# Kernel tuning notes

Measured on AMD Instinct MI355X. Metric: run time of the kernel, lower is better.

The kernel has to match this reference:

```python
import math
import jax, jax.numpy as jnp
import numpy as np

N_HEADS = 16

def setup_inputs() -> dict:
    key = jax.random.key(0)
    k1, k2, k3 = jax.random.split(key, 3)
    B, T, C = 4, 2048, 1024
    alpha = 0.5
    std = alpha * (1.0 / C) ** 0.5
    x = jax.random.normal(k1, (B, T, C), dtype=jnp.float32)
    w_attn = jax.random.normal(k2, (C, 3 * C), dtype=jnp.float32) * std
    b_attn = jnp.zeros((3 * C,), dtype=jnp.float32)
    w_proj = jax.random.normal(k3, (C, C), dtype=jnp.float32) * std
    b_proj = jnp.zeros((C,), dtype=jnp.float32)
    return {"x": x, "w_attn": w_attn, "b_attn": b_attn, "w_proj": w_proj, "b_proj": b_proj}

def reference(x, w_attn, b_attn, w_proj, b_proj):
    B, T, C = x.shape
    H = N_HEADS
    D = C // H
    qkv = x @ w_attn + b_attn                      # [B,T,3C]
    q, k, v = jnp.split(qkv, 3, axis=-1)
    # [B,T,C] -> [B,H,T,D]
    q = q.reshape(B, T, H, D).transpose(0, 2, 1, 3)
    k = k.reshape(B, T, H, D).transpose(0, 2, 1, 3)
    v = v.reshape(B, T, H, D).transpose(0, 2, 1, 3)
    att = jnp.einsum('bhqd,bhkd->bhqk', q, k) * (1.0 / math.sqrt(D))
    causal = jnp.tril(jnp.ones((T, T), dtype=bool))
    att = jnp.where(causal, att, -jnp.inf)
    att = jax.nn.softmax(att, axis=-1)
    y = jnp.einsum('bhqk,bhkd->bhqd', att, v)      # [B,H,T,D]
    y = y.transpose(0, 2, 1, 3).reshape(B, T, C)
    return y @ w_proj + b_proj
```

## Files before the change

kernel.cpp:

```cpp
#include <hip/hip_runtime.h>
#include <hip/hip_bf16.h>

typedef __bf16 bf16x8 __attribute__((ext_vector_type(8)));
typedef float f32x4 __attribute__((ext_vector_type(4)));
typedef unsigned short u16x8 __attribute__((ext_vector_type(8)));
typedef unsigned short u16x4 __attribute__((ext_vector_type(4)));

#define HB 16
#define TT 2048
#define CCH 1024
#define DD 64

#define AS1 __attribute__((address_space(1)))
#define AS3 __attribute__((address_space(3)))
#define GL16(gp, lp) __builtin_amdgcn_global_load_lds((const AS1 void*)(gp), (AS3 void*)(lp), 16, 0, 0)

__device__ __forceinline__ unsigned short f2bf(float f) {
  union { __hip_bfloat16 h; unsigned short u; } cv;
  cv.h = __float2bfloat16(f);
  return cv.u;
}

__device__ __forceinline__ unsigned pack2(float lo, float hi) {
  return (unsigned)f2bf(lo) | ((unsigned)f2bf(hi) << 16);
}

__device__ __forceinline__ f32x4 mfma16(bf16x8 a, bf16x8 b, f32x4 c) {
  return __builtin_amdgcn_mfma_f32_16x16x32_bf16(a, b, c, 0, 0, 0);
}


__global__ __launch_bounds__(256) void cvt_f32_bf16(const float* __restrict__ in,
                                                    unsigned short* __restrict__ out,
                                                    int n4) {
  int i = blockIdx.x * 256 + threadIdx.x;
  if (i >= n4) return;
  float4 v = reinterpret_cast<const float4*>(in)[i];
  u16x4 o;
  o.x = f2bf(v.x); o.y = f2bf(v.y); o.z = f2bf(v.z); o.w = f2bf(v.w);
  *reinterpret_cast<u16x4*>(out + (size_t)i * 4) = o;
}

__global__ __launch_bounds__(256) void transpose_cvt(const float* __restrict__ w,
                                                     unsigned short* __restrict__ wt,
                                                     int N) {
  __shared__ unsigned short t[32][33];
  int nb = blockIdx.x * 32, kb = blockIdx.y * 32;
  int tx = threadIdx.x & 31, ty = threadIdx.x >> 5;
  #pragma unroll
  for (int r = 0; r < 32; r += 8)
    t[ty + r][tx] = f2bf(w[(size_t)(kb + ty + r) * N + nb + tx]);
  __syncthreads();
  #pragma unroll
  for (int r = 0; r < 32; r += 8)
    wt[(size_t)(nb + ty + r) * 1024 + kb + tx] = t[tx][ty + r];
}


template <int EPI>
__global__ __launch_bounds__(256) void gemm_bf16(
    const unsigned short* __restrict__ A,
    const unsigned short* __restrict__ Bt,
    const float* __restrict__ bias,
    float* __restrict__ outf,
    unsigned short* __restrict__ qb,
    unsigned short* __restrict__ kb,
    unsigned short* __restrict__ vt) {
  __shared__ unsigned short As[8192];
  __shared__ unsigned short Bs[8192];
  const int tid = threadIdx.x;
  const int lane = tid & 63;
  const int wid = tid >> 6;
  const int r16 = lane & 15, g = lane >> 4;
  const int wm = wid >> 1, wn = wid & 1;
  const int m0 = blockIdx.y * 128, n0 = blockIdx.x * 128;
  const int srow = tid >> 3;
  const int schx = (tid & 7) ^ (srow & 7);

  f32x4 acc[4][4];
  #pragma unroll
  for (int i = 0; i < 4; ++i)
    #pragma unroll
    for (int j = 0; j < 4; ++j) acc[i][j] = (f32x4){0.f, 0.f, 0.f, 0.f};

  const int rx = r16 & 7;

  for (int kt = 0; kt < 1024; kt += 64) {
    #pragma unroll
    for (int i = 0; i < 4; ++i) {
      const int row = i * 32 + srow;
      GL16(A + (size_t)(m0 + row) * 1024 + kt + schx * 8, As + i * 2048 + tid * 8);
    }
    #pragma unroll
    for (int i = 0; i < 4; ++i) {
      const int row = i * 32 + srow;
      GL16(Bt + (size_t)(n0 + row) * 1024 + kt + schx * 8, Bs + i * 2048 + tid * 8);
    }
    __syncthreads();
    #pragma unroll
    for (int h = 0; h < 2; ++h) {
      bf16x8 af[4], bfr[4];
      #pragma unroll
      for (int i = 0; i < 4; ++i)
        af[i] = *reinterpret_cast<const bf16x8*>(
            &As[(wm * 64 + i * 16 + r16) * 64 + ((g + 4 * h) ^ rx) * 8]);
      #pragma unroll
      for (int j = 0; j < 4; ++j)
        bfr[j] = *reinterpret_cast<const bf16x8*>(
            &Bs[(wn * 64 + j * 16 + r16) * 64 + ((g + 4 * h) ^ rx) * 8]);
      #pragma unroll
      for (int i = 0; i < 4; ++i)
        #pragma unroll
        for (int j = 0; j < 4; ++j)
          acc[i][j] = mfma16(af[i], bfr[j], acc[i][j]);
    }
    __syncthreads();
  }

  #pragma unroll
  for (int i = 0; i < 4; ++i) {
    #pragma unroll
    for (int j = 0; j < 4; ++j) {
      const int n = n0 + wn * 64 + j * 16 + r16;
      const int mbase = m0 + wm * 64 + i * 16 + g * 4;
      const float bi = bias[n];
      if (EPI == 1) {
        #pragma unroll
        for (int r = 0; r < 4; ++r)
          outf[(size_t)(mbase + r) * 1024 + n] = acc[i][j][r] + bi;
      } else {
        const int which = n >> 10;
        const int cc2 = n & 1023;
        const int h = cc2 >> 6, d = cc2 & 63;
        const int b = mbase >> 11, t = mbase & 2047;
        if (which == 2) {
          u16x4 o;
          #pragma unroll
          for (int r = 0; r < 4; ++r) o[r] = f2bf(acc[i][j][r] + bi);
          *reinterpret_cast<u16x4*>(
              &vt[(((size_t)b * HB + h) * DD + d) * TT + t]) = o;
        } else {
          unsigned short* dst = (which == 0) ? qb : kb;
          const float sc = (which == 0) ? 0.18033688011112042f : 1.0f;
          #pragma unroll
          for (int r = 0; r < 4; ++r)
            dst[(((size_t)b * HB + h) * TT + (t + r)) * DD + d] =
                f2bf((acc[i][j][r] + bi) * sc);
        }
      }
    }
  }
}


__global__ __launch_bounds__(512, 2) void attn_kernel(
    const unsigned short* __restrict__ qg_,
    const unsigned short* __restrict__ kg_,
    const unsigned short* __restrict__ vtg_,
    unsigned short* __restrict__ yb) {
  const int bh = blockIdx.y;
  const int jb = blockIdx.x;
  const int tid = threadIdx.x;
  const int wid = tid >> 6;
  const int lane = tid & 63;
  const int r16 = lane & 15, g = lane >> 4;
  const unsigned short* Q = qg_ + (size_t)bh * TT * DD;
  const unsigned short* K = kg_ + (size_t)bh * TT * DD;
  const unsigned short* Vt = vtg_ + (size_t)bh * DD * TT;
  const int b = bh >> 4, h = bh & 15;

  __shared__ unsigned short smem[2][16384];

  const int krow0 = tid >> 3;
  const int kchx = (tid & 7) ^ (krow0 & 7);
  const int vd0 = tid >> 4;
  const int vchx = (tid & 15) ^ (vd0 & 7);
  const int rx = r16 & 7;

#define STAGE(bi, kvb_) do {                                                      \
    unsigned short* sb_ = &smem[bi][0];                                           \
    const unsigned short* gk_ = K + (size_t)(kvb_) * DD;                          \
    GL16(gk_ + (size_t)krow0 * DD + kchx * 8,              sb_ + tid * 8);        \
    GL16(gk_ + (size_t)(64 + krow0) * DD + kchx * 8,       sb_ + 4096 + tid * 8); \
    GL16(Vt + (size_t)vd0 * TT + (kvb_) + vchx * 8,        sb_ + 8192 + tid * 8); \
    GL16(Vt + (size_t)(32 + vd0) * TT + (kvb_) + vchx * 8, sb_ + 12288 + tid * 8);\
  } while (0)

  #pragma unroll
  for (int part = 0; part < 2; ++part) {
    const int qg0 = (part == 0) ? jb * 128 : (15 - jb) * 128;
    const int nt = (part == 0) ? (jb + 1) : (16 - jb);
    const int qw = qg0 + wid * 16;
    const int q = qw + r16;

    bf16x8 qf0 = *reinterpret_cast<const bf16x8*>(&Q[(size_t)q * DD + g * 8]);
    bf16x8 qf1 = *reinterpret_cast<const bf16x8*>(&Q[(size_t)q * DD + 32 + g * 8]);

    f32x4 yacc[4];
    #pragma unroll
    for (int db = 0; db < 4; ++db) yacc[db] = (f32x4){0.f, 0.f, 0.f, 0.f};
    float m = -1e30f, l = 0.f;

    STAGE(0, qg0 * 0);
    if (nt > 1) {
      STAGE(1, 128);
      asm volatile("s_waitcnt vmcnt(4)" ::: "memory");
    } else {
      asm volatile("s_waitcnt vmcnt(0)" ::: "memory");
    }
    __builtin_amdgcn_s_barrier();

    for (int t = 0; t < nt; ++t) {
      const int kvb = t * 128;
      const unsigned short* sK = &smem[t & 1][0];
      const unsigned short* sV = &smem[t & 1][8192];

      float s[8][4];
      #pragma unroll
      for (int c = 0; c < 8; ++c) {
        bf16x8 kfa = *reinterpret_cast<const bf16x8*>(
            &sK[(c * 16 + r16) * 64 + (g ^ rx) * 8]);
        bf16x8 kfb = *reinterpret_cast<const bf16x8*>(
            &sK[(c * 16 + r16) * 64 + ((g + 4) ^ rx) * 8]);
        f32x4 z = (f32x4){0.f, 0.f, 0.f, 0.f};
        z = mfma16(kfa, qf0, z);
        z = mfma16(kfb, qf1, z);
        #pragma unroll
        for (int r = 0; r < 4; ++r) s[c][r] = z[r];
      }

      float mx = -1e30f;
      if (t == nt - 1) {
        #pragma unroll
        for (int c = 0; c < 8; ++c)
          #pragma unroll
          for (int r = 0; r < 4; ++r) {
            if (kvb + c * 16 + 4 * g + r > q) s[c][r] = -1e30f;
            mx = fmaxf(mx, s[c][r]);
          }
      } else {
        #pragma unroll
        for (int c = 0; c < 8; ++c)
          #pragma unroll
          for (int r = 0; r < 4; ++r) mx = fmaxf(mx, s[c][r]);
      }
      mx = fmaxf(mx, __shfl_xor(mx, 16));
      mx = fmaxf(mx, __shfl_xor(mx, 32));

      if (!__all(mx <= m + 8.f)) {
        const float mn = fmaxf(m, mx);
        const float al = exp2f(m - mn);
        m = mn;
        l *= al;
        #pragma unroll
        for (int db = 0; db < 4; ++db)
          #pragma unroll
          for (int r = 0; r < 4; ++r) yacc[db][r] *= al;
      }
      float rs = 0.f;
      #pragma unroll
      for (int c = 0; c < 8; ++c)
        #pragma unroll
        for (int r = 0; r < 4; ++r) {
          s[c][r] = exp2f(s[c][r] - m);
          rs += s[c][r];
        }
      rs += __shfl_xor(rs, 16);
      rs += __shfl_xor(rs, 32);
      l += rs;

      const int s0l = r16 + 16 * ((2 * g) & 3);
      const int s1l = r16 + 16 * ((2 * g + 1) & 3);
      #pragma unroll
      for (int kk = 0; kk < 4; ++kk) {
        const unsigned x0 = pack2(s[2 * kk][0], s[2 * kk][1]);
        const unsigned x1 = pack2(s[2 * kk][2], s[2 * kk][3]);
        const unsigned y0 = pack2(s[2 * kk + 1][0], s[2 * kk + 1][1]);
        const unsigned y1 = pack2(s[2 * kk + 1][2], s[2 * kk + 1][3]);
        unsigned a0 = __shfl((int)x0, s0l, 64);
        unsigned b0 = __shfl((int)y0, s0l, 64);
        unsigned a1 = __shfl((int)x1, s0l, 64);
        unsigned b1 = __shfl((int)y1, s0l, 64);
        unsigned a2 = __shfl((int)x0, s1l, 64);
        unsigned b2 = __shfl((int)y0, s1l, 64);
        unsigned a3 = __shfl((int)x1, s1l, 64);
        unsigned b3 = __shfl((int)y1, s1l, 64);
        union { unsigned w[4]; bf16x8 v; } pf;
        pf.w[0] = (g < 2) ? a0 : b0;
        pf.w[1] = (g < 2) ? a1 : b1;
        pf.w[2] = (g < 2) ? a2 : b2;
        pf.w[3] = (g < 2) ? a3 : b3;
        #pragma unroll
        for (int db = 0; db < 4; ++db) {
          bf16x8 vf = *reinterpret_cast<const bf16x8*>(
              &sV[(db * 16 + r16) * 128 + ((kk * 4 + g) ^ rx) * 8]);
          yacc[db] = mfma16(vf, pf.v, yacc[db]);
        }
      }

      __syncthreads();
      if (t + 2 < nt) STAGE(t & 1, (t + 2) * 128);
    }

    const float rl = 1.0f / l;
    #pragma unroll
    for (int db = 0; db < 4; ++db) {
      u16x4 o;
      #pragma unroll
      for (int r = 0; r < 4; ++r) o[r] = f2bf(yacc[db][r] * rl);
      *reinterpret_cast<u16x4*>(
          &yb[((size_t)b * TT + q) * CCH + h * DD + db * 16 + 4 * g]) = o;
    }
  }
#undef STAGE
}


extern "C" void kernel_launch(void* const* d_in, const int* in_sizes, int n_in,
                              void* d_out, int out_size, void* d_ws, size_t ws_size,
                              hipStream_t stream) {
  const float* x      = (const float*)d_in[0];
  const float* w_attn = (const float*)d_in[1];
  const float* b_attn = (const float*)d_in[2];
  const float* w_proj = (const float*)d_in[3];
  const float* b_proj = (const float*)d_in[4];
  float* out = (float*)d_out;
  char* ws = (char*)d_ws;

  unsigned short* xb  = (unsigned short*)(ws + 0);
  unsigned short* wat = (unsigned short*)(ws + 16777216);
  unsigned short* wpt = (unsigned short*)(ws + 23068672);
  unsigned short* qb  = (unsigned short*)(ws + 25165824);
  unsigned short* kb  = (unsigned short*)(ws + 41943040);
  unsigned short* vt  = (unsigned short*)(ws + 58720256);
  unsigned short* yb  = (unsigned short*)(ws + 75497472);

  cvt_f32_bf16<<<(8192 * 1024 / 4 + 255) / 256, 256, 0, stream>>>(x, xb, 8192 * 1024 / 4);
  transpose_cvt<<<dim3(3072 / 32, 32), 256, 0, stream>>>(w_attn, wat, 3072);
  transpose_cvt<<<dim3(1024 / 32, 32), 256, 0, stream>>>(w_proj, wpt, 1024);

  gemm_bf16<0><<<dim3(3072 / 128, 8192 / 128), 256, 0, stream>>>(
      xb, wat, b_attn, nullptr, qb, kb, vt);

  attn_kernel<<<dim3(8, 4 * HB), 512, 0, stream>>>(qb, kb, vt, yb);

  gemm_bf16<1><<<dim3(1024 / 128, 8192 / 128), 256, 0, stream>>>(
      yb, wpt, b_proj, out, nullptr, nullptr, nullptr);
}
```

Baseline: 194.8 us.

## Shrink attention tiles to 64 queries and 64 keys with 4-wave blocks

```diff
diff --git a/kernel.cpp b/kernel.cpp
--- a/kernel.cpp
+++ b/kernel.cpp
@@ -153,7 +153,7 @@
 }
 
 
-__global__ __launch_bounds__(512, 2) void attn_kernel(
+__global__ __launch_bounds__(256, 4) void attn_kernel(
     const unsigned short* __restrict__ qg_,
     const unsigned short* __restrict__ kg_,
     const unsigned short* __restrict__ vtg_,
@@ -169,27 +169,25 @@
   const unsigned short* Vt = vtg_ + (size_t)bh * DD * TT;
   const int b = bh >> 4, h = bh & 15;
 
-  __shared__ unsigned short smem[2][16384];
+  __shared__ unsigned short smem[2][8192];
 
   const int krow0 = tid >> 3;
-  const int kchx = (tid & 7) ^ (krow0 & 7);
-  const int vd0 = tid >> 4;
-  const int vchx = (tid & 15) ^ (vd0 & 7);
+  const int chx = (tid & 7) ^ (krow0 & 7);
   const int rx = r16 & 7;
 
-#define STAGE(bi, kvb_) do {                                                      \
-    unsigned short* sb_ = &smem[bi][0];                                           \
-    const unsigned short* gk_ = K + (size_t)(kvb_) * DD;                          \
-    GL16(gk_ + (size_t)krow0 * DD + kchx * 8,              sb_ + tid * 8);        \
-    GL16(gk_ + (size_t)(64 + krow0) * DD + kchx * 8,       sb_ + 4096 + tid * 8); \
-    GL16(Vt + (size_t)vd0 * TT + (kvb_) + vchx * 8,        sb_ + 8192 + tid * 8); \
-    GL16(Vt + (size_t)(32 + vd0) * TT + (kvb_) + vchx * 8, sb_ + 12288 + tid * 8);\
+#define STAGE(bi, kvb_) do {                                                    \
+    unsigned short* sb_ = &smem[bi][0];                                         \
+    const unsigned short* gk_ = K + (size_t)(kvb_) * DD;                        \
+    GL16(gk_ + (size_t)krow0 * DD + chx * 8,               sb_ + tid * 8);      \
+    GL16(gk_ + (size_t)(32 + krow0) * DD + chx * 8,        sb_ + 2048 + tid * 8);\
+    GL16(Vt + (size_t)krow0 * TT + (kvb_) + chx * 8,       sb_ + 4096 + tid * 8);\
+    GL16(Vt + (size_t)(32 + krow0) * TT + (kvb_) + chx * 8, sb_ + 6144 + tid * 8);\
   } while (0)
 
   #pragma unroll
   for (int part = 0; part < 2; ++part) {
-    const int qg0 = (part == 0) ? jb * 128 : (15 - jb) * 128;
-    const int nt = (part == 0) ? (jb + 1) : (16 - jb);
+    const int qg0 = (part == 0) ? jb * 64 : (31 - jb) * 64;
+    const int nt = (part == 0) ? (jb + 1) : (32 - jb);
     const int qw = qg0 + wid * 16;
     const int q = qw + r16;
 
@@ -201,9 +199,9 @@
     for (int db = 0; db < 4; ++db) yacc[db] = (f32x4){0.f, 0.f, 0.f, 0.f};
     float m = -1e30f, l = 0.f;
 
-    STAGE(0, qg0 * 0);
+    STAGE(0, 0);
     if (nt > 1) {
-      STAGE(1, 128);
+      STAGE(1, 64);
       asm volatile("s_waitcnt vmcnt(4)" ::: "memory");
     } else {
       asm volatile("s_waitcnt vmcnt(0)" ::: "memory");
@@ -211,13 +209,13 @@
     __builtin_amdgcn_s_barrier();
 
     for (int t = 0; t < nt; ++t) {
-      const int kvb = t * 128;
+      const int kvb = t * 64;
       const unsigned short* sK = &smem[t & 1][0];
-      const unsigned short* sV = &smem[t & 1][8192];
-
-      float s[8][4];
-      #pragma unroll
-      for (int c = 0; c < 8; ++c) {
+      const unsigned short* sV = &smem[t & 1][4096];
+
+      float s[4][4];
+      #pragma unroll
+      for (int c = 0; c < 4; ++c) {
         bf16x8 kfa = *reinterpret_cast<const bf16x8*>(
             &sK[(c * 16 + r16) * 64 + (g ^ rx) * 8]);
         bf16x8 kfb = *reinterpret_cast<const bf16x8*>(
@@ -229,21 +227,18 @@
         for (int r = 0; r < 4; ++r) s[c][r] = z[r];
       }
 
-      float mx = -1e30f;
       if (t == nt - 1) {
         #pragma unroll
-        for (int c = 0; c < 8; ++c)
+        for (int c = 0; c < 4; ++c)
           #pragma unroll
-          for (int r = 0; r < 4; ++r) {
+          for (int r = 0; r < 4; ++r)
             if (kvb + c * 16 + 4 * g + r > q) s[c][r] = -1e30f;
-            mx = fmaxf(mx, s[c][r]);
-          }
-      } else {
-        #pragma unroll
-        for (int c = 0; c < 8; ++c)
-          #pragma unroll
-          for (int r = 0; r < 4; ++r) mx = fmaxf(mx, s[c][r]);
-      }
+      }
+      float mc[4];
+      #pragma unroll
+      for (int c = 0; c < 4; ++c)
+        mc[c] = fmaxf(fmaxf(s[c][0], s[c][1]), fmaxf(s[c][2], s[c][3]));
+      float mx = fmaxf(fmaxf(mc[0], mc[1]), fmaxf(mc[2], mc[3]));
       mx = fmaxf(mx, __shfl_xor(mx, 16));
       mx = fmaxf(mx, __shfl_xor(mx, 32));
 
@@ -257,14 +252,14 @@
           #pragma unroll
           for (int r = 0; r < 4; ++r) yacc[db][r] *= al;
       }
-      float rs = 0.f;
-      #pragma unroll
-      for (int c = 0; c < 8; ++c)
-        #pragma unroll
-        for (int r = 0; r < 4; ++r) {
-          s[c][r] = exp2f(s[c][r] - m);
-          rs += s[c][r];
-        }
+      float sc4[4];
+      #pragma unroll
+      for (int c = 0; c < 4; ++c) {
+        #pragma unroll
+        for (int r = 0; r < 4; ++r) s[c][r] = exp2f(s[c][r] - m);
+        sc4[c] = (s[c][0] + s[c][1]) + (s[c][2] + s[c][3]);
+      }
+      float rs = (sc4[0] + sc4[1]) + (sc4[2] + sc4[3]);
       rs += __shfl_xor(rs, 16);
       rs += __shfl_xor(rs, 32);
       l += rs;
@@ -272,7 +267,7 @@
       const int s0l = r16 + 16 * ((2 * g) & 3);
       const int s1l = r16 + 16 * ((2 * g + 1) & 3);
       #pragma unroll
-      for (int kk = 0; kk < 4; ++kk) {
+      for (int kk = 0; kk < 2; ++kk) {
         const unsigned x0 = pack2(s[2 * kk][0], s[2 * kk][1]);
         const unsigned x1 = pack2(s[2 * kk][2], s[2 * kk][3]);
         const unsigned y0 = pack2(s[2 * kk + 1][0], s[2 * kk + 1][1]);
@@ -293,13 +288,13 @@
         #pragma unroll
         for (int db = 0; db < 4; ++db) {
           bf16x8 vf = *reinterpret_cast<const bf16x8*>(
-              &sV[(db * 16 + r16) * 128 + ((kk * 4 + g) ^ rx) * 8]);
+              &sV[(db * 16 + r16) * 64 + ((kk * 4 + g) ^ rx) * 8]);
           yacc[db] = mfma16(vf, pf.v, yacc[db]);
         }
       }
 
       __syncthreads();
-      if (t + 2 < nt) STAGE(t & 1, (t + 2) * 128);
+      if (t + 2 < nt) STAGE(t & 1, (t + 2) * 64);
     }
 
     const float rl = 1.0f / l;
@@ -342,7 +337,7 @@
   gemm_bf16<0><<<dim3(3072 / 128, 8192 / 128), 256, 0, stream>>>(
       xb, wat, b_attn, nullptr, qb, kb, vt);
 
-  attn_kernel<<<dim3(8, 4 * HB), 512, 0, stream>>>(qb, kb, vt, yb);
+  attn_kernel<<<dim3(16, 4 * HB), 256, 0, stream>>>(qb, kb, vt, yb);
 
   gemm_bf16<1><<<dim3(1024 / 128, 8192 / 128), 256, 0, stream>>>(
       yb, wpt, b_proj, out, nullptr, nullptr, nullptr);
```

New measurement: 199.5 us. +2.4%, slower.
